# Optimization experiments

Measured on AMD Instinct MI355X. Metric: run time of the kernel, lower is better.

The kernel has to match this reference:

```python
import jax, jax.numpy as jnp
import numpy as np

P_RATE = 0.2      # perturbation_rate
N_PERT = 100      # num_perturbations
EPS = 1e-6


def setup_inputs() -> dict:
    key = jax.random.key(0)
    k1, k2 = jax.random.split(key)
    B, D = 1024, 512
    return {
        "spatial_features": jax.random.normal(k1, (B, D), dtype=jnp.float32),
        "spectral_features": jax.random.normal(k2, (B, D), dtype=jnp.float32),
    }


def _perturb_all(key, features):
    # Vectorized over all N_PERT perturbations at once.
    # torch.std(dim=1) uses Bessel correction (ddof=1), per-sample scalar.
    km, kn = jax.random.split(key)
    P = N_PERT
    shape = (P,) + features.shape                      # [P, B, D]
    mask = (jax.random.uniform(km, shape) < P_RATE).astype(features.dtype)
    std = jnp.std(features, axis=1, keepdims=True, ddof=1)  # [B, 1]
    noise = jax.random.normal(kn, shape, dtype=features.dtype) * std
    return features[None] + mask * noise               # [P, B, D]


def reference(spatial_features, spectral_features):
    key = jax.random.key(42)
    k_spa, k_spe = jax.random.split(key)
    pert_spa = _perturb_all(k_spa, spatial_features)   # [P, B, D]
    pert_spe = _perturb_all(k_spe, spectral_features)  # [P, B, D]
    candidates = jnp.concatenate([pert_spa, pert_spe], axis=2)  # [P, B, 2D]

    # Dynamic weighted fusion: variance over perturbation axis (unbiased=False)
    var = jnp.var(candidates, axis=0) + EPS            # [B, 2D]
    weight = 1.0 / var
    weight = weight / jnp.sum(weight, axis=0, keepdims=True)  # normalize over batch (faithful to source)
    Z = jnp.sum(candidates * weight[None], axis=0)     # [B, 2D]
    return Z
```

## Files before the change

### kernel.cpp

```cpp
#include <hip/hip_runtime.h>
#include <stdint.h>

#define B 1024
#define D 512
#define NPERT 100
#define BD (B * D)
#define QBD (BD / 4)
#define C2 (2 * D)
#define OUT_N (B * C2)

#define MASK_THR 858993664u

__host__ __device__ __forceinline__ uint32_t rotl32(uint32_t v, int r) {
    return (v << r) | (v >> (32 - r));
}

__host__ __device__ __forceinline__ void tf2x32(uint32_t k0, uint32_t k1,
                                                uint32_t x0, uint32_t x1,
                                                uint32_t& o0, uint32_t& o1) {
    uint32_t ks2 = k0 ^ k1 ^ 0x1BD11BDAu;
    x0 += k0; x1 += k1;
#define TF_R4(a,b,c,d_) \
    x0 += x1; x1 = rotl32(x1, a); x1 ^= x0; \
    x0 += x1; x1 = rotl32(x1, b); x1 ^= x0; \
    x0 += x1; x1 = rotl32(x1, c); x1 ^= x0; \
    x0 += x1; x1 = rotl32(x1, d_); x1 ^= x0;
    TF_R4(13, 15, 26, 6);  x0 += k1;  x1 += ks2 + 1u;
    TF_R4(17, 29, 16, 24); x0 += ks2; x1 += k0  + 2u;
    TF_R4(13, 15, 26, 6);  x0 += k0;  x1 += k1  + 3u;
    TF_R4(17, 29, 16, 24); x0 += k1;  x1 += ks2 + 4u;
    TF_R4(13, 15, 26, 6);  x0 += ks2; x1 += k0  + 5u;
#undef TF_R4
    o0 = x0; o1 = x1;
}

static void host_child(uint32_t k0, uint32_t k1, uint32_t i,
                       uint32_t& c0, uint32_t& c1) {
    tf2x32(k0, k1, 0u, i, c0, c1);
}

__device__ __forceinline__ uint32_t pbits32(uint32_t k0, uint32_t k1, uint32_t j) {
    uint32_t b0, b1;
    tf2x32(k0, k1, 0u, j, b0, b1);
    return b0 ^ b1;
}

__device__ __forceinline__ float normal_from_bits(uint32_t bits) {
    const float lo = -0.99999994f;
    float f = __uint_as_float((bits >> 9) | 0x3F800000u) - 1.0f;
    float u = fmaf(f, 2.0f, lo);
    float w = -0.69314718f * __builtin_amdgcn_logf(fmaf(-u, u, 1.0f));
    float p;
    if (__builtin_expect(w >= 5.0f, 0)) {
        float s = sqrtf(w) - 3.0f;
        p = -0.00028314702f;
        p = fmaf(p, s, 0.00014276567f);
        p = fmaf(p, s, 0.0019082633f);
        p = fmaf(p, s, -0.0051950082f);
        p = fmaf(p, s, 0.0081169485f);
        p = fmaf(p, s, -0.010779902f);
        p = fmaf(p, s, 0.013348609f);
        p = fmaf(p, s, 1.4165813f);
        p = fmaf(p, s, 4.0064936f);
    } else {
        float t = w - 2.5f;
        p = 3.9742444e-08f;
        p = fmaf(p, t, 4.8546906e-07f);
        p = fmaf(p, t, -4.9828437e-06f);
        p = fmaf(p, t, -6.2105324e-06f);
        p = fmaf(p, t, 0.00030912052f);
        p = fmaf(p, t, -0.0017730336f);
        p = fmaf(p, t, -0.0059081636f);
        p = fmaf(p, t, 0.34880054f);
        p = fmaf(p, t, 2.1233180f);
    }
    return p * u;
}

__device__ float g_std[2 * B];
__device__ float g_inv[OUT_N];
__device__ float g_part[16 * C2];
__device__ float g_colsum[C2];

__global__ void std_kernel(const float* __restrict__ spa,
                           const float* __restrict__ spe) {
    int row = blockIdx.x;
    const float* x = (row < B) ? (spa + row * D) : (spe + (row - B) * D);
    int t = threadIdx.x;
    float s = 0.0f, s2 = 0.0f;
    #pragma unroll
    for (int k = 0; k < D / 64; ++k) {
        float v = x[t + 64 * k];
        s += v;
        s2 += v * v;
    }
    #pragma unroll
    for (int off = 32; off > 0; off >>= 1) {
        s  += __shfl_down(s, off);
        s2 += __shfl_down(s2, off);
    }
    if (t == 0) {
        float var = (s2 - s * s * (1.0f / (float)D)) * (1.0f / (float)(D - 1));
        g_std[row] = sqrtf(fmaxf(var, 0.0f));
    }
}

__global__ __launch_bounds__(256) void main_kernel(
        const float* __restrict__ spa, const float* __restrict__ spe,
        float* __restrict__ out,
        uint32_t kmA0, uint32_t kmA1, uint32_t knA0, uint32_t knA1,
        uint32_t kmB0, uint32_t kmB1, uint32_t knB0, uint32_t knB1) {
    int feat = (int)(blockIdx.x >> 9);
    int idx  = (int)((blockIdx.x & 511u) * 256u + threadIdx.x);

    uint32_t km0 = feat ? kmB0 : kmA0;
    uint32_t km1 = feat ? kmB1 : kmA1;
    uint32_t kn0 = feat ? knB0 : knA0;
    uint32_t kn1 = feat ? knB1 : knA1;

    const float* src = feat ? spe : spa;

    float x[4], sd[4], T1[4], T2[4];
    uint32_t j[4];
    #pragma unroll
    for (int e = 0; e < 4; ++e) {
        int rem = idx + e * QBD;
        x[e]  = src[rem];
        sd[e] = g_std[feat * B + (rem >> 9)];
        j[e]  = (uint32_t)rem;
        T1[e] = 0.0f;
        T2[e] = 0.0f;
    }

    #pragma unroll 1
    for (int p = 0; p < NPERT; ++p) {
        uint32_t mb[4], nb[4];
        #pragma unroll
        for (int e = 0; e < 4; ++e) {
            mb[e] = pbits32(km0, km1, j[e]);
            nb[e] = pbits32(kn0, kn1, j[e]);
            j[e] += BD;
        }
        #pragma unroll
        for (int e = 0; e < 4; ++e) {
            float n = normal_from_bits(nb[e]);
            float g = (mb[e] < MASK_THR) ? n : 0.0f;
            T1[e] += g;
            T2[e] = fmaf(g, g, T2[e]);
        }
    }

    #pragma unroll
    for (int e = 0; e < 4; ++e) {
        int rem = idx + e * QBD;
        float S   = 100.0f * x[e] + sd[e] * T1[e];
        float mu  = T1[e] * 0.01f;
        float var = sd[e] * sd[e] * (T2[e] * 0.01f - mu * mu) + 1e-6f;
        float inv = 1.0f / var;
        int c = (feat << 9) | (rem & (D - 1));
        int o = (rem >> 9) * C2 + c;
        g_inv[o] = inv;
        out[o]   = inv * S;
    }
}

__global__ void colsum_part_kernel() {
    int c = blockIdx.x * 256 + threadIdx.x;
    int grp = blockIdx.y;
    const float* base = g_inv + grp * 64 * C2 + c;
    float s = 0.0f;
    #pragma unroll 4
    for (int r = 0; r < 64; ++r) s += base[r * C2];
    g_part[grp * C2 + c] = s;
}

__global__ void colsum_fin_kernel() {
    int c = blockIdx.x * 256 + threadIdx.x;
    float s = 0.0f;
    #pragma unroll
    for (int g = 0; g < 16; ++g) s += g_part[g * C2 + c];
    g_colsum[c] = s;
}

__global__ void finalize_kernel(float* __restrict__ out) {
    int i = blockIdx.x * 256 + threadIdx.x;
    out[i] = out[i] / g_colsum[i & (C2 - 1)];
}

extern "C" void kernel_launch(void* const* d_in, const int* in_sizes, int n_in,
                              void* d_out, int out_size, void* d_ws, size_t ws_size,
                              hipStream_t stream) {
    const float* spa = (const float*)d_in[0];
    const float* spe = (const float*)d_in[1];
    float* out = (float*)d_out;

    uint32_t spa0, spa1, spe0, spe1;
    host_child(0u, 42u, 0u, spa0, spa1);
    host_child(0u, 42u, 1u, spe0, spe1);
    uint32_t ka[4], kb[4];
    host_child(spa0, spa1, 0u, ka[0], ka[1]);
    host_child(spa0, spa1, 1u, ka[2], ka[3]);
    host_child(spe0, spe1, 0u, kb[0], kb[1]);
    host_child(spe0, spe1, 1u, kb[2], kb[3]);

    std_kernel<<<2 * B, 64, 0, stream>>>(spa, spe);

    main_kernel<<<1024, 256, 0, stream>>>(
        spa, spe, out,
        ka[0], ka[1], ka[2], ka[3],
        kb[0], kb[1], kb[2], kb[3]);

    dim3 pgrid(4, 16);
    colsum_part_kernel<<<pgrid, 256, 0, stream>>>();
    colsum_fin_kernel<<<4, 256, 0, stream>>>();
    finalize_kernel<<<OUT_N / 256, 256, 0, stream>>>(out);
}
```

Baseline: 413.1 us.

## Split perturbation loop across two block halves and combine partial sums

The main kernel now splits the 100 perturbations into two halves handled by separate blocks, doubling the grid from 1024 to 2048 blocks. Each block writes partial (T1, T2) sums to a global buffer. A new combine kernel adds the halves and computes the variance, inverse weight and output. This aims to raise occupancy and CU utilisation on a GPU with many CUs, at the cost of an extra kernel launch and roughly 8 MB of extra global traffic.

Result: faster. 404.3 us (-2.1%).

```diff
diff --git a/kernel.cpp b/kernel.cpp
--- a/kernel.cpp
+++ b/kernel.cpp
@@ -78,6 +78,7 @@
 }
 
 __device__ float g_std[2 * B];
+__device__ float2 g_pp[2][2 * BD];
 __device__ float g_inv[OUT_N];
 __device__ float g_part[16 * C2];
 __device__ float g_colsum[C2];
@@ -106,11 +107,10 @@
 }
 
 __global__ __launch_bounds__(256) void main_kernel(
-        const float* __restrict__ spa, const float* __restrict__ spe,
-        float* __restrict__ out,
         uint32_t kmA0, uint32_t kmA1, uint32_t knA0, uint32_t knA1,
         uint32_t kmB0, uint32_t kmB1, uint32_t knB0, uint32_t knB1) {
-    int feat = (int)(blockIdx.x >> 9);
+    int feat = (int)(blockIdx.x >> 10);
+    int half = (int)((blockIdx.x >> 9) & 1u);
     int idx  = (int)((blockIdx.x & 511u) * 256u + threadIdx.x);
 
     uint32_t km0 = feat ? kmB0 : kmA0;
@@ -118,22 +118,18 @@
     uint32_t kn0 = feat ? knB0 : knA0;
     uint32_t kn1 = feat ? knB1 : knA1;
 
-    const float* src = feat ? spe : spa;
-
-    float x[4], sd[4], T1[4], T2[4];
+    uint32_t jbase = (uint32_t)idx + (uint32_t)half * (NPERT / 2) * BD;
+    float T1[4], T2[4];
     uint32_t j[4];
     #pragma unroll
     for (int e = 0; e < 4; ++e) {
-        int rem = idx + e * QBD;
-        x[e]  = src[rem];
-        sd[e] = g_std[feat * B + (rem >> 9)];
-        j[e]  = (uint32_t)rem;
+        j[e]  = jbase + e * QBD;
         T1[e] = 0.0f;
         T2[e] = 0.0f;
     }
 
     #pragma unroll 1
-    for (int p = 0; p < NPERT; ++p) {
+    for (int p = 0; p < NPERT / 2; ++p) {
         uint32_t mb[4], nb[4];
         #pragma unroll
         for (int e = 0; e < 4; ++e) {
@@ -152,16 +148,30 @@
 
     #pragma unroll
     for (int e = 0; e < 4; ++e) {
-        int rem = idx + e * QBD;
-        float S   = 100.0f * x[e] + sd[e] * T1[e];
-        float mu  = T1[e] * 0.01f;
-        float var = sd[e] * sd[e] * (T2[e] * 0.01f - mu * mu) + 1e-6f;
-        float inv = 1.0f / var;
-        int c = (feat << 9) | (rem & (D - 1));
-        int o = (rem >> 9) * C2 + c;
-        g_inv[o] = inv;
-        out[o]   = inv * S;
-    }
+        g_pp[half][feat * BD + idx + e * QBD] = make_float2(T1[e], T2[e]);
+    }
+}
+
+__global__ void combine_kernel(const float* __restrict__ spa,
+                               const float* __restrict__ spe,
+                               float* __restrict__ out) {
+    int elem = blockIdx.x * 256 + threadIdx.x;
+    int feat = elem >> 19;
+    int rem  = elem & (BD - 1);
+    float2 pa = g_pp[0][elem];
+    float2 pb = g_pp[1][elem];
+    float T1 = pa.x + pb.x;
+    float T2 = pa.y + pb.y;
+    const float* src = feat ? spe : spa;
+    float x  = src[rem];
+    float sd = g_std[feat * B + (rem >> 9)];
+    float S   = 100.0f * x + sd * T1;
+    float mu  = T1 * 0.01f;
+    float var = sd * sd * (T2 * 0.01f - mu * mu) + 1e-6f;
+    float inv = 1.0f / var;
+    int o = (rem >> 9) * C2 + ((feat << 9) | (rem & (D - 1)));
+    g_inv[o] = inv;
+    out[o]   = inv * S;
 }
 
 __global__ void colsum_part_kernel() {
@@ -205,10 +215,11 @@
 
     std_kernel<<<2 * B, 64, 0, stream>>>(spa, spe);
 
-    main_kernel<<<1024, 256, 0, stream>>>(
-        spa, spe, out,
+    main_kernel<<<2048, 256, 0, stream>>>(
         ka[0], ka[1], ka[2], ka[3],
         kb[0], kb[1], kb[2], kb[3]);
+
+    combine_kernel<<<(2 * BD) / 256, 256, 0, stream>>>(spa, spe, out);
 
     dim3 pgrid(4, 16);
     colsum_part_kernel<<<pgrid, 256, 0, stream>>>();
```
